# Kernel tuning notes

Measured on AMD Instinct MI355X. Metric: run time of the kernel, lower is better.

Reference implementation:

```python
import jax, jax.numpy as jnp
import numpy as np

EPS = 1e-5

def _bn(x, g, b):
    # training-mode BatchNorm3d over (N, T, H, W) per channel (axis=1), biased variance
    red = (0, 2, 3, 4)
    m = x.mean(red, keepdims=True)
    v = x.var(red, keepdims=True)
    s = (1, -1, 1, 1, 1)
    return (x - m) / jnp.sqrt(v + EPS) * g.reshape(s) + b.reshape(s)

def _conv3d(x, w, b):
    # Conv3d kernel (1,3,3), padding (0,1,1)
    y = jax.lax.conv_general_dilated(x, w, (1, 1, 1), ((0, 0), (1, 1), (1, 1)),
                                     dimension_numbers=('NCDHW', 'OIDHW', 'NCDHW'))
    return y + b[None, :, None, None, None]

def _forward(x1, x2, attn_weight, W_up, b_up, W_mlp, b_mlp, g_mlp, be_mlp,
             W_c1, b_c1, g_c1, be_c1, W_c2, b_c2, g_c2, be_c2):
    w2 = W_up[:, :, 0]  # [Cin, Cout, 2, 2]
    y = jnp.einsum('bcthw,cokl->bothkwl', x1, w2)
    b_, o, t, h, k, w_, l = y.shape
    x1u = y.reshape(b_, o, t, h * k, w_ * l) + b_up[None, :, None, None, None]

    bs, d_in, T, H, W = x2.shape
    nH = attn_weight.shape[0]
    hh, ww = attn_weight.shape[2], attn_weight.shape[3]
    # [nH, bs, h, w, T, T] -> [nH*bs, T*T, h, w], bilinear upsample to (H, W)
    A = attn_weight.transpose(0, 1, 4, 5, 2, 3).reshape(nH * bs, T * T, hh, ww)
    A = jax.image.resize(A, (nH * bs, T * T, H, W), method='linear')
    A = A.reshape(nH, bs, T, T, H, W)
    # per-(head,b,H,W) temporal attention matmul: avoids materializing x2.repeat(n_head,...)
    ctx = jnp.einsum('nbtsxy,bcsxy->btxycn', A, x2)  # [bs,T,H,W,d_in,nH]
    ctx = ctx.reshape(bs, T, H, W, d_in * nH)        # flatten order (c, n) matches torch permute+view
    hmlp = jnp.einsum('btxyk,ko->btxyo', ctx, W_mlp) + b_mlp
    hmlp = hmlp.transpose(0, 4, 1, 2, 3)  # [bs, enc, T, H, W]
    hmlp = jax.nn.relu(_bn(hmlp, g_mlp, be_mlp))

    x = jnp.concatenate([hmlp, x1u], axis=1)  # [bs, enc+dec, T, H, W]
    x = jax.nn.relu(_bn(_conv3d(x, W_c1, b_c1), g_c1, be_c1))
    x = jax.nn.relu(_bn(_conv3d(x, W_c2, b_c2), g_c2, be_c2))
    return x

def setup_inputs() -> dict:
    key = jax.random.key(0)
    ks = jax.random.split(key, 8)
    bs, T, H, W = 2, 8, 128, 128
    dec, enc, nH = 64, 32, 4
    hh = ww = 16  # attn_scale_factor = 8
    return {
        'x1': jax.random.normal(ks[0], (bs, dec, T, H // 2, W // 2), jnp.float32),
        'x2': jax.random.normal(ks[1], (bs, enc, T, H, W), jnp.float32),
        'attn_weight': jax.random.uniform(ks[2], (nH, bs, hh, ww, T, T), jnp.float32),
        'W_up': jax.random.normal(ks[3], (dec, dec, 1, 2, 2), jnp.float32) * 0.05,
        'b_up': jnp.zeros((dec,), jnp.float32),
        'W_mlp': jax.random.normal(ks[4], (nH * enc, enc), jnp.float32) * 0.05,
        'b_mlp': jnp.zeros((enc,), jnp.float32),
        'g_mlp': jnp.ones((enc,), jnp.float32),
        'be_mlp': jnp.zeros((enc,), jnp.float32),
        'W_c1': jax.random.normal(ks[5], (enc, dec + enc, 1, 3, 3), jnp.float32) * 0.05,
        'b_c1': jnp.zeros((enc,), jnp.float32),
        'g_c1': jnp.ones((enc,), jnp.float32),
        'be_c1': jnp.zeros((enc,), jnp.float32),
        'W_c2': jax.random.normal(ks[6], (enc, enc, 1, 3, 3), jnp.float32) * 0.05,
        'b_c2': jnp.zeros((enc,), jnp.float32),
        'g_c2': jnp.ones((enc,), jnp.float32),
        'be_c2': jnp.zeros((enc,), jnp.float32),
    }

def reference(x1, x2, attn_weight, W_up, b_up, W_mlp, b_mlp, g_mlp, be_mlp,
              W_c1, b_c1, g_c1, be_c1, W_c2, b_c2, g_c2, be_c2):
    return _forward(x1, x2, attn_weight, W_up, b_up, W_mlp, b_mlp, g_mlp, be_mlp,
                    W_c1, b_c1, g_c1, be_c1, W_c2, b_c2, g_c2, be_c2)
```

## Files before the change

### kernel.cpp

```cpp
#include <hip/hip_runtime.h>


#define EPSV 1e-5f

typedef __attribute__((ext_vector_type(8))) short short8;
typedef __attribute__((ext_vector_type(4))) short short4v;
typedef __attribute__((ext_vector_type(4))) float floatx4;

__device__ inline short f2bf(float f) {
  union { float f; unsigned u; } v; v.f = f;
  unsigned r = (v.u + 0x7fffu + ((v.u >> 16) & 1u)) >> 16;
  return (short)r;
}
__device__ inline float bf2f(short s) {
  union { unsigned u; float f; } v; v.u = ((unsigned)(unsigned short)s) << 16;
  return v.f;
}

#define UB_OFF   0
#define HMB_OFF  8388608
#define C1B_OFF  12582912
#define C2B_OFF  16777216
#define X2B_OFF  20971520
#define WB1_OFF  25165824
#define WB2_OFF  25179648
#define WUP_OFF  25184256
#define ST_OFF   25192448
#define SC_OFF   25192640

__global__ __launch_bounds__(256) void k_repackb(const float* __restrict__ Wc1, const float* __restrict__ Wc2,
        const float* __restrict__ Wup,
        short* __restrict__ wb1, short* __restrict__ wb2, short* __restrict__ wupb) {
  int i = blockIdx.x*256 + threadIdx.x;
  if (i < 27648) {
    int cc = i / 9216, r = i % 9216;
    int tap = r / 1024, r2 = r % 1024;
    int nt = r2 >> 9, lane = (r2 >> 3) & 63, j = r2 & 7;
    int o = nt*16 + (lane & 15);
    int cin = cc*32 + (lane >> 4)*8 + j;
    wb1[i] = f2bf(Wc1[(o*96 + cin)*9 + tap]);
  }
  if (i < 9216) {
    int tap = i / 1024, r2 = i % 1024;
    int nt = r2 >> 9, lane = (r2 >> 3) & 63, j = r2 & 7;
    int o = nt*16 + (lane & 15);
    int cin = (lane >> 4)*8 + j;
    wb2[i] = f2bf(Wc2[(o*32 + cin)*9 + tap]);
  }
  if (i < 16384) {
    int j = i & 7, lane = (i >> 3) & 63, r = i >> 9;
    int nt = r & 3, kb = (r >> 2) & 1, p = r >> 3;
    int c = kb*32 + (lane >> 4)*8 + j;
    int o = nt*16 + (lane & 15);
    wupb[i] = f2bf(Wup[(c*64 + o)*4 + p]);
  }
}

__global__ __launch_bounds__(256) void k_x2b(const float* __restrict__ x2, short* __restrict__ x2b) {
  long i = ((long)blockIdx.x*256 + threadIdx.x)*4;
  float4 v = *(const float4*)(x2 + i);
  short4v o;
  o[0]=f2bf(v.x); o[1]=f2bf(v.y); o[2]=f2bf(v.z); o[3]=f2bf(v.w);
  *(short4v*)(x2b + i) = o;
}

__global__ __launch_bounds__(256) void k_up_mfma(const float* __restrict__ x1,
        const short* __restrict__ wupb, const float* __restrict__ bup,
        short* __restrict__ Ub) {
  __shared__ __align__(16) char smem[34816];
  short8* stage = (short8*)smem;
  int t = blockIdx.y, b = blockIdx.z;
  int chunk = blockIdx.x >> 2, parity = blockIdx.x & 3;
  int tid = threadIdx.x, lane = tid & 63, w = tid >> 6;

  {
    const float* xp = x1 + ((long)(b*64)*8 + t)*4096 + chunk*256 + tid;
    #pragma unroll
    for (int o8 = 0; o8 < 8; ++o8) {
      short8 v;
      #pragma unroll
      for (int j = 0; j < 8; ++j) v[j] = f2bf(xp[(long)(o8*8+j)*32768]);
      int kb = o8 >> 2, cq = o8 & 3;
      stage[(kb*16 + (tid>>4))*64 + cq*16 + (tid&15)] = v;
    }
  }
  __syncthreads();

  floatx4 acc[4][4];
  #pragma unroll
  for (int nt=0; nt<4; ++nt) {
    float bb = bup[nt*16 + (lane&15)];
    #pragma unroll
    for (int mt=0; mt<4; ++mt) acc[mt][nt] = (floatx4){bb,bb,bb,bb};
  }
  const short8* wp = (const short8*)wupb;
  #pragma unroll
  for (int kb=0; kb<2; ++kb) {
    short8 bfr[4];
    #pragma unroll
    for (int nt=0; nt<4; ++nt) bfr[nt] = wp[((parity*2+kb)*4+nt)*64 + lane];
    #pragma unroll
    for (int mt=0; mt<4; ++mt) {
      short8 a = stage[(kb*16 + w*4 + mt)*64 + lane];
      #pragma unroll
      for (int nt=0; nt<4; ++nt)
        acc[mt][nt] = __builtin_amdgcn_mfma_f32_16x16x32_bf16(a, bfr[nt], acc[mt][nt], 0,0,0);
    }
  }

  __syncthreads();
  short* trb = (short*)smem;
  #pragma unroll
  for (int mt=0; mt<4; ++mt)
    #pragma unroll
    for (int nt=0; nt<4; ++nt)
      #pragma unroll
      for (int r=0; r<4; ++r)
        trb[(w*64 + mt*16 + (lane>>4)*4 + r)*68 + nt*16 + (lane&15)] = f2bf(acc[mt][nt][r]);
  __syncthreads();

  int ip = chunk*256 + tid;
  int X = 2*(ip>>6) + (parity>>1), Y = 2*(ip&63) + (parity&1);
  short* dst = Ub + (((long)(b*8+t)*16384 + X*128 + Y)*64);
  const short* src = trb + tid*68;
  #pragma unroll
  for (int k=0; k<16; ++k)
    *(short4v*)(dst + k*4) = *(const short4v*)(src + k*4);
}

__global__ __launch_bounds__(256) void k_ctxmlp(const short* __restrict__ x2b,
        const float* __restrict__ attn, const float* __restrict__ Wmlp,
        const float* __restrict__ bmlp, short* __restrict__ HMb, float* __restrict__ st) {
  __shared__ float la[8448];
  __shared__ float sb[64];
  int t = blockIdx.y, b = blockIdx.z;
  int tid = threadIdx.x, lane = tid & 63;
  int pos = blockIdx.x*256 + tid;
  if (tid < 64) sb[tid] = 0.f;
  float4* la4 = (float4*)la;
  const float4* g4 = (const float4*)attn;
  #pragma unroll
  for (int k=0;k<8;++k) {
    int i = k*256 + tid;
    int s4 = i & 1, iy = (i>>1)&15, ix = (i>>5)&15, n = i>>9;
    la4[i] = g4[((((n*2+b)*16+ix)*16+iy)*8+t)*2 + s4];
  }
  __syncthreads();
  int x = pos >> 7, y = pos & 127;
  float ux = (x+0.5f)*0.125f - 0.5f;
  float uy = (y+0.5f)*0.125f - 0.5f;
  int ix0 = (int)floorf(ux), iy0 = (int)floorf(uy);
  float fx = ux - (float)ix0, fy = uy - (float)iy0;
  int ixa = max(ix0,0), ixb = min(ix0+1,15);
  int iya = max(iy0,0), iyb = min(iy0+1,15);
  float w00=(1.f-fx)*(1.f-fy), w01=(1.f-fx)*fy, w10=fx*(1.f-fy), w11=fx*fy;
  float a[4][8];
  #pragma unroll
  for (int n=0;n<4;++n) {
    const float4* p00 = la4 + ((n*16+ixa)*16+iya)*2;
    const float4* p01 = la4 + ((n*16+ixa)*16+iyb)*2;
    const float4* p10 = la4 + ((n*16+ixb)*16+iya)*2;
    const float4* p11 = la4 + ((n*16+ixb)*16+iyb)*2;
    #pragma unroll
    for (int q=0;q<2;++q) {
      float4 c00=p00[q], c01=p01[q], c10=p10[q], c11=p11[q];
      a[n][q*4+0] = w00*c00.x + w01*c01.x + w10*c10.x + w11*c11.x;
      a[n][q*4+1] = w00*c00.y + w01*c01.y + w10*c10.y + w11*c11.y;
      a[n][q*4+2] = w00*c00.z + w01*c01.z + w10*c10.z + w11*c11.z;
      a[n][q*4+3] = w00*c00.w + w01*c01.w + w10*c10.w + w11*c11.w;
    }
  }
  float acc[32];
  #pragma unroll
  for (int o=0;o<32;++o) acc[o] = bmlp[o];
  const short* x2p = x2b + (long)b*4194304 + pos;
  #pragma unroll 4
  for (int c=0;c<32;++c) {
    float xr[8];
    #pragma unroll
    for (int s=0;s<8;++s) xr[s] = bf2f(x2p[(long)(c*8+s)*16384]);
    #pragma unroll
    for (int n=0;n<4;++n) {
      float ctx = 0.f;
      #pragma unroll
      for (int s=0;s<8;++s) ctx = fmaf(a[n][s], xr[s], ctx);
      const float* wrow = Wmlp + (c*4+n)*32;
      #pragma unroll
      for (int o=0;o<32;++o) acc[o] = fmaf(ctx, wrow[o], acc[o]);
    }
  }
  short8* hp = (short8*)(HMb + ((long)((b*8+t)*16384 + pos)) * 32);
  #pragma unroll
  for (int g=0; g<4; ++g) {
    short8 v;
    #pragma unroll
    for (int j=0;j<8;++j) v[j] = f2bf(acc[g*8+j]);
    hp[g] = v;
  }
  __syncthreads();
  #pragma unroll
  for (int c=0;c<32;++c) la[tid*33 + c] = acc[c];
  __syncthreads();
  int ch = tid & 31, grp = tid >> 5;
  float s = 0.f, q = 0.f;
  #pragma unroll 8
  for (int p=0;p<32;++p) { float v = la[(grp*32+p)*33 + ch]; s += v; q += v*v; }
  s += __shfl_xor(s, 32); q += __shfl_xor(q, 32);
  if (lane < 32) { atomicAdd(&sb[ch], s); atomicAdd(&sb[32+ch], q); }
  __syncthreads();
  if (tid < 64) atomicAdd(&st[tid], sb[tid]);
}

__global__ void k_finalize(const float* __restrict__ st, const float* __restrict__ g,
                           const float* __restrict__ be, float* __restrict__ sc, float* __restrict__ sh) {
  int c = threadIdx.x;
  if (c < 32) {
    float mean = st[c] * (1.f/262144.f);
    float var  = st[32+c] * (1.f/262144.f) - mean*mean;
    float s = g[c] / sqrtf(var + EPSV);
    sc[c] = s;
    sh[c] = be[c] - mean*s;
  }
}

template<int NCHUNK>
__global__ __launch_bounds__(256) void k_convp(
    const short* __restrict__ src0, const short* __restrict__ srcU,
    const short* __restrict__ wb, const float* __restrict__ bias,
    const float* __restrict__ sc, const float* __restrict__ sh,
    short* __restrict__ dstCL, float* __restrict__ st) {
  constexpr int NBUF = (NCHUNK > 1) ? 2 : 1;
  __shared__ __align__(16) short stage[NBUF][324*40];
  __shared__ float sbuf[64];
  int t = blockIdx.y, b = blockIdx.z;
  int tid = threadIdx.x, lane = tid & 63, w = tid >> 6;
  if (tid < 64) sbuf[tid] = 0.f;
  long slab = (long)(b*8+t)*16384;
  int x0 = (int)(blockIdx.x >> 3) * 16, y0 = (int)(blockIdx.x & 7) * 16;
  int m = lane & 15, kg = lane >> 4;

  int pA = tid;        int rA = pA/18, cA = pA - rA*18;
  int XA = x0-1+rA, YA = y0-1+cA;
  bool okA = ((unsigned)XA < 128u) & ((unsigned)YA < 128u);
  int pB = tid + 256;  bool hasB = pB < 324;
  int rB = pB/18, cB = pB - rB*18;
  int XB = x0-1+rB, YB = y0-1+cB;
  bool okB = hasB && (((unsigned)XB < 128u) & ((unsigned)YB < 128u));
  long offA = slab + XA*128 + YA, offB = slab + XB*128 + YB;

  short8 preA[4], preB[4];

  float bias0 = bias[m], bias1 = bias[16 + m];
  floatx4 acc[4][2];
  #pragma unroll
  for (int mt=0; mt<4; ++mt) {
    acc[mt][0] = (floatx4){bias0,bias0,bias0,bias0};
    acc[mt][1] = (floatx4){bias1,bias1,bias1,bias1};
  }

  {
    const short* sA = src0 + offA*32;
    const short* sB = src0 + offB*32;
    #pragma unroll
    for (int g=0; g<4; ++g) {
      preA[g] = okA ? *(const short8*)(sA + g*8) : (short8)0;
      preB[g] = okB ? *(const short8*)(sB + g*8) : (short8)0;
    }
  }
  #pragma unroll
  for (int g=0; g<4; ++g) {
    short8 vA, vB;
    #pragma unroll
    for (int j=0;j<8;++j) {
      int ch = g*8+j;
      float scv = sc[ch], shv = sh[ch];
      vA[j] = okA ? f2bf(fmaxf(fmaf(bf2f(preA[g][j]), scv, shv), 0.f)) : (short)0;
      vB[j] = okB ? f2bf(fmaxf(fmaf(bf2f(preB[g][j]), scv, shv), 0.f)) : (short)0;
    }
    *(short8*)(&stage[0][pA*40 + g*8]) = vA;
    if (hasB) *(short8*)(&stage[0][pB*40 + g*8]) = vB;
  }
  __syncthreads();

  const short8* wbp = (const short8*)wb;
  #pragma unroll
  for (int cc=0; cc<NCHUNK; ++cc) {
    if (cc+1 < NCHUNK) {
      int coff = cc*32;
      const short* sA = srcU + offA*64 + coff;
      const short* sB = srcU + offB*64 + coff;
      #pragma unroll
      for (int g=0; g<4; ++g) {
        preA[g] = okA ? *(const short8*)(sA + g*8) : (short8)0;
        preB[g] = okB ? *(const short8*)(sB + g*8) : (short8)0;
      }
    }
    #pragma unroll
    for (int tap=0; tap<9; ++tap) {
      int dy = tap/3, dx = tap - 3*dy;
      short8 b0 = wbp[((cc*9+tap)*2+0)*64 + lane];
      short8 b1 = wbp[((cc*9+tap)*2+1)*64 + lane];
      #pragma unroll
      for (int mt=0; mt<4; ++mt) {
        int p = (w*4 + mt + dy)*18 + m + dx;
        short8 a = *(const short8*)(&stage[cc & (NBUF-1)][p*40 + kg*8]);
        acc[mt][0] = __builtin_amdgcn_mfma_f32_16x16x32_bf16(a, b0, acc[mt][0], 0,0,0);
        acc[mt][1] = __builtin_amdgcn_mfma_f32_16x16x32_bf16(a, b1, acc[mt][1], 0,0,0);
      }
    }
    if (cc+1 < NCHUNK) {
      #pragma unroll
      for (int g=0; g<4; ++g) {
        *(short8*)(&stage[(cc+1) & (NBUF-1)][pA*40 + g*8]) = preA[g];
        if (hasB) *(short8*)(&stage[(cc+1) & (NBUF-1)][pB*40 + g*8]) = preB[g];
      }
    }
    __syncthreads();
  }

  float s0=0.f,q0=0.f,s1=0.f,q1=0.f;
  #pragma unroll
  for (int mt=0; mt<4; ++mt)
    #pragma unroll
    for (int r=0; r<4; ++r) {
      float v0 = acc[mt][0][r]; s0 += v0; q0 += v0*v0;
      float v1 = acc[mt][1][r]; s1 += v1; q1 += v1*v1;
    }
  s0 += __shfl_xor(s0,16); s0 += __shfl_xor(s0,32);
  q0 += __shfl_xor(q0,16); q0 += __shfl_xor(q0,32);
  s1 += __shfl_xor(s1,16); s1 += __shfl_xor(s1,32);
  q1 += __shfl_xor(q1,16); q1 += __shfl_xor(q1,32);
  if (lane < 16) {
    atomicAdd(&sbuf[lane],    s0); atomicAdd(&sbuf[16+lane], s1);
    atomicAdd(&sbuf[32+lane], q0); atomicAdd(&sbuf[48+lane], q1);
  }

  short* tr = &stage[0][0];
  #pragma unroll
  for (int mt=0; mt<4; ++mt) {
    int tile = w*4 + mt;
    #pragma unroll
    for (int nt=0; nt<2; ++nt)
      #pragma unroll
      for (int r=0; r<4; ++r) {
        int pin = kg*4 + r;
        tr[(tile*16 + pin)*32 + nt*16 + m] = f2bf(acc[mt][nt][r]);
      }
  }
  __syncthreads();
  int px = tid >> 4, py = tid & 15;
  short8* d8 = (short8*)(dstCL + ((slab + (long)(x0+px)*128 + (y0+py))*32));
  const short8* s8 = (const short8*)(tr + tid*32);
  d8[0]=s8[0]; d8[1]=s8[1]; d8[2]=s8[2]; d8[3]=s8[3];
  if (tid < 64) atomicAdd(&st[tid], sbuf[tid]);
}

__global__ __launch_bounds__(256) void k_bnrelu2(const short* __restrict__ C2b,
        const float* __restrict__ sc, const float* __restrict__ sh,
        float* __restrict__ out) {
  __shared__ float tb[10592];
  int t = blockIdx.y, b = blockIdx.z;
  int posbase = blockIdx.x * 256;
  int tid = threadIdx.x;
  long slab = (long)(b*8+t)*16384;
  {
    const short8* sp = (const short8*)(C2b + (slab + posbase + tid)*32);
    int pi = tid + (tid>>5)*8;
    #pragma unroll
    for (int g=0; g<4; ++g) {
      short8 v = sp[g];
      #pragma unroll
      for (int j=0; j<8; ++j) {
        int ch = g*8+j;
        tb[ch*321 + pi] = fmaxf(fmaf(bf2f(v[j]), sc[ch], sh[ch]), 0.f);
      }
    }
  }
  __syncthreads();
  int ch = tid >> 3, pg = tid & 7;
  float* op = out + ((long)(b*32+ch)*8 + t)*16384 + posbase + pg*32;
  const float* tp = tb + ch*321 + pg*40;
  #pragma unroll
  for (int k=0; k<8; ++k) {
    float4 v;
    v.x = tp[k*4+0]; v.y = tp[k*4+1]; v.z = tp[k*4+2]; v.w = tp[k*4+3];
    *(float4*)(op + k*4) = v;
  }
}

extern "C" void kernel_launch(void* const* d_in, const int* in_sizes, int n_in,
                              void* d_out, int out_size, void* d_ws, size_t ws_size,
                              hipStream_t stream) {
  (void)in_sizes; (void)n_in; (void)out_size; (void)ws_size;
  const float* x1   = (const float*)d_in[0];
  const float* x2   = (const float*)d_in[1];
  const float* attn = (const float*)d_in[2];
  const float* Wup  = (const float*)d_in[3];
  const float* bup  = (const float*)d_in[4];
  const float* Wmlp = (const float*)d_in[5];
  const float* bmlp = (const float*)d_in[6];
  const float* gmlp = (const float*)d_in[7];
  const float* bemlp= (const float*)d_in[8];
  const float* Wc1  = (const float*)d_in[9];
  const float* bc1  = (const float*)d_in[10];
  const float* gc1  = (const float*)d_in[11];
  const float* bec1 = (const float*)d_in[12];
  const float* Wc2  = (const float*)d_in[13];
  const float* bc2  = (const float*)d_in[14];
  const float* gc2  = (const float*)d_in[15];
  const float* bec2 = (const float*)d_in[16];
  float* ws  = (float*)d_ws;
  float* out = (float*)d_out;

  short* Ub   = (short*)(ws + UB_OFF);
  short* HMb  = (short*)(ws + HMB_OFF);
  short* C1b  = (short*)(ws + C1B_OFF);
  short* C2b  = (short*)(ws + C2B_OFF);
  short* x2b  = (short*)(ws + X2B_OFF);
  short* wb1  = (short*)(ws + WB1_OFF);
  short* wb2  = (short*)(ws + WB2_OFF);
  short* wupb = (short*)(ws + WUP_OFF);
  float* st1  = ws + ST_OFF;
  float* st2  = st1 + 64;
  float* st3  = st2 + 64;
  float* sc1  = ws + SC_OFF;  float* sh1 = sc1+32;
  float* sc2  = sh1+32;       float* sh2 = sc2+32;
  float* sc3  = sh2+32;       float* sh3 = sc3+32;

  hipMemsetAsync(st1, 0, 192*sizeof(float), stream);
  k_repackb<<<108, 256, 0, stream>>>(Wc1, Wc2, Wup, wb1, wb2, wupb);
  k_x2b<<<8192, 256, 0, stream>>>(x2, x2b);
  k_up_mfma<<<dim3(64,8,2), 256, 0, stream>>>(x1, wupb, bup, Ub);
  k_ctxmlp<<<dim3(64,8,2), 256, 0, stream>>>(x2b, attn, Wmlp, bmlp, HMb, st1);
  k_finalize<<<1, 32, 0, stream>>>(st1, gmlp, bemlp, sc1, sh1);
  k_convp<3><<<dim3(64,8,2), 256, 0, stream>>>(HMb, Ub, wb1, bc1, sc1, sh1, C1b, st2);
  k_finalize<<<1, 32, 0, stream>>>(st2, gc1, bec1, sc2, sh2);
  k_convp<1><<<dim3(64,8,2), 256, 0, stream>>>(C1b, nullptr, wb2, bc2, sc2, sh2, C2b, st3);
  k_finalize<<<1, 32, 0, stream>>>(st3, gc2, bec2, sc3, sh3);
  k_bnrelu2<<<dim3(64,8,2), 256, 0, stream>>>(C2b, sc3, sh3, out);
}
```

Before: 323.6 us.

## Move MLP projection in ctx kernel to bf16 MFMA with channel-last x2

Replaces the scalar per-thread 128x32 MLP FMA loop in the context kernel with bf16 MFMA tiles. Per-pixel context values are staged through LDS and the MLP weights are pre-packed into MFMA fragment order. x2 is now transposed to a channel-last bf16 layout so each pixel's channels load as vectors. The attention tile loaded into LDS is also reduced to only the rows the block needs. The intent is to cut VALU work and scattered global loads, at the cost of an extra bf16 rounding of the context values and more block barriers.

After: 308.0 us. 1.05x faster.

```diff
diff --git a/kernel.cpp b/kernel.cpp
--- a/kernel.cpp
+++ b/kernel.cpp
@@ -21,16 +21,17 @@
 #define HMB_OFF  8388608
 #define C1B_OFF  12582912
 #define C2B_OFF  16777216
-#define X2B_OFF  20971520
-#define WB1_OFF  25165824
-#define WB2_OFF  25179648
-#define WUP_OFF  25184256
-#define ST_OFF   25192448
-#define SC_OFF   25192640
+#define X2T_OFF  20971520
+#define WB1_OFF  29360128
+#define WB2_OFF  29373952
+#define WUP_OFF  29378560
+#define WMB_OFF  29386752
+#define ST_OFF   29388800
+#define SC_OFF   29388992
 
 __global__ __launch_bounds__(256) void k_repackb(const float* __restrict__ Wc1, const float* __restrict__ Wc2,
-        const float* __restrict__ Wup,
-        short* __restrict__ wb1, short* __restrict__ wb2, short* __restrict__ wupb) {
+        const float* __restrict__ Wup, const float* __restrict__ Wmlp,
+        short* __restrict__ wb1, short* __restrict__ wb2, short* __restrict__ wupb, short* __restrict__ wmb) {
   int i = blockIdx.x*256 + threadIdx.x;
   if (i < 27648) {
     int cc = i / 9216, r = i % 9216;
@@ -54,14 +55,37 @@
     int o = nt*16 + (lane & 15);
     wupb[i] = f2bf(Wup[(c*64 + o)*4 + p]);
   }
-}
-
-__global__ __launch_bounds__(256) void k_x2b(const float* __restrict__ x2, short* __restrict__ x2b) {
-  long i = ((long)blockIdx.x*256 + threadIdx.x)*4;
-  float4 v = *(const float4*)(x2 + i);
-  short4v o;
-  o[0]=f2bf(v.x); o[1]=f2bf(v.y); o[2]=f2bf(v.z); o[3]=f2bf(v.w);
-  *(short4v*)(x2b + i) = o;
+  if (i < 4096) {
+    int j = i & 7, lane = (i >> 3) & 63, nt = (i >> 9) & 1, ck = i >> 10;
+    int k = ck*32 + (lane >> 4)*8 + j;
+    int o = nt*16 + (lane & 15);
+    wmb[i] = f2bf(Wmlp[k*32 + o]);
+  }
+}
+
+__global__ __launch_bounds__(256) void k_x2t(const float* __restrict__ x2, short* __restrict__ x2t) {
+  __shared__ short lds[32*264];
+  int s = blockIdx.y, b = blockIdx.z;
+  int tile = blockIdx.x;
+  int tid = threadIdx.x;
+  #pragma unroll
+  for (int k=0; k<8; ++k) {
+    int f4 = k*256 + tid;
+    int c = f4 >> 6, p4 = f4 & 63;
+    float4 v = *(const float4*)(x2 + ((long)(b*32+c)*8 + s)*16384 + tile*256 + p4*4);
+    short4v o;
+    o[0]=f2bf(v.x); o[1]=f2bf(v.y); o[2]=f2bf(v.z); o[3]=f2bf(v.w);
+    *(short4v*)(lds + c*264 + p4*4) = o;
+  }
+  __syncthreads();
+  short* dst = x2t + (((long)(b*8+s)*16384) + tile*256 + tid)*32;
+  #pragma unroll
+  for (int g=0; g<4; ++g) {
+    short8 v;
+    #pragma unroll
+    for (int j=0; j<8; ++j) v[j] = lds[(g*8+j)*264 + tid];
+    *(short8*)(dst + g*8) = v;
+  }
 }
 
 __global__ __launch_bounds__(256) void k_up_mfma(const float* __restrict__ x1,
@@ -128,39 +152,48 @@
     *(short4v*)(dst + k*4) = *(const short4v*)(src + k*4);
 }
 
-__global__ __launch_bounds__(256) void k_ctxmlp(const short* __restrict__ x2b,
-        const float* __restrict__ attn, const float* __restrict__ Wmlp,
+__global__ __launch_bounds__(256) void k_ctxmlp(const short* __restrict__ x2t,
+        const float* __restrict__ attn, const short* __restrict__ wmb,
         const float* __restrict__ bmlp, short* __restrict__ HMb, float* __restrict__ st) {
-  __shared__ float la[8448];
+  __shared__ float la[2048];
+  __shared__ __align__(16) short ctxs[256*40];
   __shared__ float sb[64];
   int t = blockIdx.y, b = blockIdx.z;
-  int tid = threadIdx.x, lane = tid & 63;
+  int tid = threadIdx.x, lane = tid & 63, w = tid >> 6;
+  int m = lane & 15, kg = lane >> 4;
   int pos = blockIdx.x*256 + tid;
   if (tid < 64) sb[tid] = 0.f;
+
+  int x0 = blockIdx.x*2;
+  int ixbase = max((int)floorf((x0+0.5f)*0.125f - 0.5f), 0);
+
   float4* la4 = (float4*)la;
   const float4* g4 = (const float4*)attn;
   #pragma unroll
-  for (int k=0;k<8;++k) {
-    int i = k*256 + tid;
-    int s4 = i & 1, iy = (i>>1)&15, ix = (i>>5)&15, n = i>>9;
-    la4[i] = g4[((((n*2+b)*16+ix)*16+iy)*8+t)*2 + s4];
-  }
-  __syncthreads();
+  for (int k=0;k<2;++k) {
+    int f = k*256 + tid;
+    int s4 = f & 1, iy = (f>>1)&15, slot = (f>>5)&3, n = f>>7;
+    int ixs = min(ixbase + slot, 15);
+    la4[f] = g4[((((n*2+b)*16+ixs)*16+iy)*8+t)*2 + s4];
+  }
+  __syncthreads();
+
   int x = pos >> 7, y = pos & 127;
   float ux = (x+0.5f)*0.125f - 0.5f;
   float uy = (y+0.5f)*0.125f - 0.5f;
   int ix0 = (int)floorf(ux), iy0 = (int)floorf(uy);
   float fx = ux - (float)ix0, fy = uy - (float)iy0;
-  int ixa = max(ix0,0), ixb = min(ix0+1,15);
+  int sa  = max(ix0,0) - ixbase;
+  int sbl = min(ix0+1,15) - ixbase;
   int iya = max(iy0,0), iyb = min(iy0+1,15);
   float w00=(1.f-fx)*(1.f-fy), w01=(1.f-fx)*fy, w10=fx*(1.f-fy), w11=fx*fy;
   float a[4][8];
   #pragma unroll
   for (int n=0;n<4;++n) {
-    const float4* p00 = la4 + ((n*16+ixa)*16+iya)*2;
-    const float4* p01 = la4 + ((n*16+ixa)*16+iyb)*2;
-    const float4* p10 = la4 + ((n*16+ixb)*16+iya)*2;
-    const float4* p11 = la4 + ((n*16+ixb)*16+iyb)*2;
+    const float4* p00 = la4 + ((n*4+sa )*16+iya)*2;
+    const float4* p01 = la4 + ((n*4+sa )*16+iyb)*2;
+    const float4* p10 = la4 + ((n*4+sbl)*16+iya)*2;
+    const float4* p11 = la4 + ((n*4+sbl)*16+iyb)*2;
     #pragma unroll
     for (int q=0;q<2;++q) {
       float4 c00=p00[q], c01=p01[q], c10=p10[q], c11=p11[q];
@@ -170,44 +203,87 @@
       a[n][q*4+3] = w00*c00.w + w01*c01.w + w10*c10.w + w11*c11.w;
     }
   }
-  float acc[32];
-  #pragma unroll
-  for (int o=0;o<32;++o) acc[o] = bmlp[o];
-  const short* x2p = x2b + (long)b*4194304 + pos;
-  #pragma unroll 4
-  for (int c=0;c<32;++c) {
-    float xr[8];
-    #pragma unroll
-    for (int s=0;s<8;++s) xr[s] = bf2f(x2p[(long)(c*8+s)*16384]);
-    #pragma unroll
-    for (int n=0;n<4;++n) {
-      float ctx = 0.f;
-      #pragma unroll
-      for (int s=0;s<8;++s) ctx = fmaf(a[n][s], xr[s], ctx);
-      const float* wrow = Wmlp + (c*4+n)*32;
-      #pragma unroll
-      for (int o=0;o<32;++o) acc[o] = fmaf(ctx, wrow[o], acc[o]);
-    }
-  }
-  short8* hp = (short8*)(HMb + ((long)((b*8+t)*16384 + pos)) * 32);
-  #pragma unroll
-  for (int g=0; g<4; ++g) {
-    short8 v;
-    #pragma unroll
-    for (int j=0;j<8;++j) v[j] = f2bf(acc[g*8+j]);
-    hp[g] = v;
-  }
-  __syncthreads();
-  #pragma unroll
-  for (int c=0;c<32;++c) la[tid*33 + c] = acc[c];
-  __syncthreads();
-  int ch = tid & 31, grp = tid >> 5;
-  float s = 0.f, q = 0.f;
-  #pragma unroll 8
-  for (int p=0;p<32;++p) { float v = la[(grp*32+p)*33 + ch]; s += v; q += v*v; }
-  s += __shfl_xor(s, 32); q += __shfl_xor(q, 32);
-  if (lane < 32) { atomicAdd(&sb[ch], s); atomicAdd(&sb[32+ch], q); }
-  __syncthreads();
+
+  float b0v = bmlp[m], b1v = bmlp[16+m];
+  floatx4 acc[4][2];
+  #pragma unroll
+  for (int mt=0; mt<4; ++mt) {
+    acc[mt][0] = (floatx4){b0v,b0v,b0v,b0v};
+    acc[mt][1] = (floatx4){b1v,b1v,b1v,b1v};
+  }
+
+  const short8* wm = (const short8*)wmb;
+  for (int ck=0; ck<4; ++ck) {
+    short8 xr[8];
+    #pragma unroll
+    for (int s=0;s<8;++s)
+      xr[s] = *(const short8*)(x2t + (((long)(b*8+s)*16384) + pos)*32 + ck*8);
+    float ctx[8][4];
+    #pragma unroll
+    for (int c=0;c<8;++c) { ctx[c][0]=0.f; ctx[c][1]=0.f; ctx[c][2]=0.f; ctx[c][3]=0.f; }
+    #pragma unroll
+    for (int s=0;s<8;++s) {
+      float xv[8];
+      #pragma unroll
+      for (int c=0;c<8;++c) xv[c] = bf2f(xr[s][c]);
+      #pragma unroll
+      for (int n=0;n<4;++n) {
+        float an = a[n][s];
+        #pragma unroll
+        for (int c=0;c<8;++c) ctx[c][n] = fmaf(an, xv[c], ctx[c][n]);
+      }
+    }
+    #pragma unroll
+    for (int g=0; g<4; ++g) {
+      short8 v;
+      #pragma unroll
+      for (int j=0;j<8;++j) { int kl = g*8+j; v[j] = f2bf(ctx[kl>>2][kl&3]); }
+      *(short8*)(ctxs + tid*40 + g*8) = v;
+    }
+    __syncthreads();
+    short8 wb0 = wm[(ck*2+0)*64 + lane];
+    short8 wb1f = wm[(ck*2+1)*64 + lane];
+    #pragma unroll
+    for (int mt=0; mt<4; ++mt) {
+      short8 af = *(const short8*)(ctxs + ((w*4+mt)*16 + m)*40 + kg*8);
+      acc[mt][0] = __builtin_amdgcn_mfma_f32_16x16x32_bf16(af, wb0,  acc[mt][0], 0,0,0);
+      acc[mt][1] = __builtin_amdgcn_mfma_f32_16x16x32_bf16(af, wb1f, acc[mt][1], 0,0,0);
+    }
+    __syncthreads();
+  }
+
+  float s0=0.f,q0=0.f,s1=0.f,q1=0.f;
+  #pragma unroll
+  for (int mt=0; mt<4; ++mt)
+    #pragma unroll
+    for (int r=0; r<4; ++r) {
+      float v0 = acc[mt][0][r]; s0 += v0; q0 += v0*v0;
+      float v1 = acc[mt][1][r]; s1 += v1; q1 += v1*v1;
+    }
+  s0 += __shfl_xor(s0,16); s0 += __shfl_xor(s0,32);
+  q0 += __shfl_xor(q0,16); q0 += __shfl_xor(q0,32);
+  s1 += __shfl_xor(s1,16); s1 += __shfl_xor(s1,32);
+  q1 += __shfl_xor(q1,16); q1 += __shfl_xor(q1,32);
+  if (lane < 16) {
+    atomicAdd(&sb[lane],    s0); atomicAdd(&sb[16+lane], s1);
+    atomicAdd(&sb[32+lane], q0); atomicAdd(&sb[48+lane], q1);
+  }
+
+  short* tr = ctxs;
+  #pragma unroll
+  for (int mt=0; mt<4; ++mt) {
+    int tile = w*4 + mt;
+    #pragma unroll
+    for (int nt=0; nt<2; ++nt)
+      #pragma unroll
+      for (int r=0; r<4; ++r)
+        tr[(tile*16 + kg*4 + r)*32 + nt*16 + m] = f2bf(acc[mt][nt][r]);
+  }
+  __syncthreads();
+  long slab = (long)(b*8+t)*16384;
+  short8* d8 = (short8*)(HMb + (slab + blockIdx.x*256 + tid)*32);
+  const short8* s8 = (const short8*)(tr + tid*32);
+  d8[0]=s8[0]; d8[1]=s8[1]; d8[2]=s8[2]; d8[3]=s8[3];
   if (tid < 64) atomicAdd(&st[tid], sb[tid]);
 }
 
@@ -342,10 +418,8 @@
     #pragma unroll
     for (int nt=0; nt<2; ++nt)
       #pragma unroll
-      for (int r=0; r<4; ++r) {
-        int pin = kg*4 + r;
-        tr[(tile*16 + pin)*32 + nt*16 + m] = f2bf(acc[mt][nt][r]);
-      }
+      for (int r=0; r<4; ++r)
+        tr[(tile*16 + kg*4 + r)*32 + nt*16 + m] = f2bf(acc[mt][nt][r]);
   }
   __syncthreads();
   int px = tid >> 4, py = tid & 15;
@@ -416,10 +490,11 @@
   short* HMb  = (short*)(ws + HMB_OFF);
   short* C1b  = (short*)(ws + C1B_OFF);
   short* C2b  = (short*)(ws + C2B_OFF);
-  short* x2b  = (short*)(ws + X2B_OFF);
+  short* x2t  = (short*)(ws + X2T_OFF);
   short* wb1  = (short*)(ws + WB1_OFF);
   short* wb2  = (short*)(ws + WB2_OFF);
   short* wupb = (short*)(ws + WUP_OFF);
+  short* wmb  = (short*)(ws + WMB_OFF);
   float* st1  = ws + ST_OFF;
   float* st2  = st1 + 64;
   float* st3  = st2 + 64;
@@ -428,10 +503,10 @@
   float* sc3  = sh2+32;       float* sh3 = sc3+32;
 
   hipMemsetAsync(st1, 0, 192*sizeof(float), stream);
-  k_repackb<<<108, 256, 0, stream>>>(Wc1, Wc2, Wup, wb1, wb2, wupb);
-  k_x2b<<<8192, 256, 0, stream>>>(x2, x2b);
+  k_repackb<<<108, 256, 0, stream>>>(Wc1, Wc2, Wup, Wmlp, wb1, wb2, wupb, wmb);
+  k_x2t<<<dim3(64,8,2), 256, 0, stream>>>(x2, x2t);
   k_up_mfma<<<dim3(64,8,2), 256, 0, stream>>>(x1, wupb, bup, Ub);
-  k_ctxmlp<<<dim3(64,8,2), 256, 0, stream>>>(x2b, attn, Wmlp, bmlp, HMb, st1);
+  k_ctxmlp<<<dim3(64,8,2), 256, 0, stream>>>(x2t, attn, wmb, bmlp, HMb, st1);
   k_finalize<<<1, 32, 0, stream>>>(st1, gmlp, bemlp, sc1, sh1);
   k_convp<3><<<dim3(64,8,2), 256, 0, stream>>>(HMb, Ub, wb1, bc1, sc1, sh1, C1b, st2);
   k_finalize<<<1, 32, 0, stream>>>(st2, gc1, bec1, sc2, sh2);
```
